# Optimization experiments

Measured on AMD Instinct MI355X. Metric: run time of the kernel, lower is better.

## Reference

```python
import jax, jax.numpy as jnp
import numpy as np

B, T, DIM, H, D = 4, 2048, 1024, 8, 128
HDIM = H * D


def _rope_tables(t, head_dim):
    # angular_freq: (1/1024)^linspace(0,1,D/4) concatenated with D/4 zeros -> length D/2
    freq = (1.0 / 1024.0) ** jnp.linspace(0.0, 1.0, head_dim // 4)
    freq = jnp.concatenate([freq.astype(jnp.float32), jnp.zeros(head_dim // 4, jnp.float32)])
    theta = jnp.arange(t, dtype=jnp.float32)[:, None] * freq[None, :]  # [T, D/2]
    return jnp.cos(theta), jnp.sin(theta)


def _rms_norm(x):
    # F.rms_norm with no weight, default eps = finfo(dtype).eps
    eps = jnp.finfo(jnp.float32).eps
    return x * jax.lax.rsqrt(jnp.mean(x * x, axis=-1, keepdims=True) + eps)


def _rope(x, cos, sin):
    # x: [B,T,H,D]; rotate-half form matching the torch module
    x1, x2 = jnp.split(x, 2, axis=-1)
    c = cos[None, :, None, :]
    s = sin[None, :, None, :]
    return jnp.concatenate([x1 * c + x2 * s, -x1 * s + x2 * c], axis=-1)


def setup_inputs() -> dict:
    key = jax.random.key(0)
    k0, k1, k2, k3 = jax.random.split(key, 4)
    std = 0.5 * DIM ** -0.5
    bound = (3.0 ** 0.5) * std
    x = jax.random.normal(k0, (B, T, DIM), jnp.float32)
    ve = jax.random.normal(k1, (B, T, HDIM), jnp.float32)
    qkv_w = jax.random.uniform(k2, (3, HDIM, DIM), jnp.float32, -bound, bound)
    lambdas = jnp.array([0.5, 0.5], jnp.float32)
    # c_proj is zero-initialized in the module; use small random weight so output is nontrivial
    c_proj_w = jax.random.uniform(k3, (DIM, HDIM), jnp.float32, -bound, bound)
    return {"x": x, "ve": ve, "qkv_w": qkv_w, "lambdas": lambdas, "c_proj_w": c_proj_w}


def reference(x, ve, qkv_w, lambdas, c_proj_w):
    b, t, dim = x.shape
    hdim = qkv_w.shape[1]
    h, d = hdim // 128, 128
    # fused QKV projection (no bias)
    qkv = (x @ qkv_w.reshape(3 * hdim, dim).T).reshape(b, t, 3 * h, d)
    q, k, v = qkv[:, :, :h], qkv[:, :, h:2 * h], qkv[:, :, 2 * h:]
    # QK RMSNorm then RoPE
    q, k = _rms_norm(q), _rms_norm(k)
    cos, sin = _rope_tables(t, d)
    q, k = _rope(q, cos, sin), _rope(k, cos, sin)
    # lambda-weighted value-embedding mix
    v = lambdas[0] * v + lambdas[1] * ve.reshape(b, t, h, d)
    # naive attention with explicit causal mask (masked_fill -1e9)
    scores = jnp.einsum('bqhd,bkhd->bhqk', q, k) * (d ** -0.5)
    causal = jnp.triu(jnp.ones((t, t), bool), k=1)  # True above diagonal
    scores = jnp.where(causal[None, None], jnp.float32(-1e9), scores)
    probs = jax.nn.softmax(scores, axis=-1)
    y = jnp.einsum('bhqk,bkhd->bqhd', probs, v).reshape(b, t, hdim)
    return y @ c_proj_w.T
```

## Files before the change

### kernel.cpp

```cpp
#include <hip/hip_runtime.h>
#include <hip/hip_bf16.h>

constexpr int B_ = 4;
constexpr int T_ = 2048;
constexpr int DIM_ = 1024;
constexpr int H_ = 8;
constexpr int D_ = 128;
constexpr int HDIM_ = H_ * D_;

typedef __attribute__((ext_vector_type(8))) short bf16x8;
typedef __attribute__((ext_vector_type(8))) unsigned short ushort8;
typedef __attribute__((ext_vector_type(4))) float f32x4;

#define ATTN_SCALE 0.08838834764831845f

__device__ __forceinline__ unsigned short f2bf(float x) {
    unsigned u = __float_as_uint(x);
    unsigned r = (u + 0x7FFFu + ((u >> 16) & 1u)) >> 16;
    return (unsigned short)r;
}
__device__ __forceinline__ float bf2f(unsigned short u) {
    return __uint_as_float(((unsigned)u) << 16);
}

__device__ __forceinline__ void async_ld16(void* ldsdst, const void* gsrc) {
    __builtin_amdgcn_global_load_lds(
        (const __attribute__((address_space(1))) unsigned int*)gsrc,
        (__attribute__((address_space(3))) unsigned int*)ldsdst, 16, 0, 0);
}

__global__ __launch_bounds__(256) void cvtk(const float* __restrict__ in,
                                            unsigned short* __restrict__ out, int n4) {
    int i = blockIdx.x * 256 + threadIdx.x;
    if (i < n4) {
        float4 v = ((const float4*)in)[i];
        ushort4 o;
        o.x = f2bf(v.x); o.y = f2bf(v.y); o.z = f2bf(v.z); o.w = f2bf(v.w);
        ((ushort4*)out)[i] = o;
    }
}

__global__ void rope_tables_k(float* __restrict__ cost, float* __restrict__ sint) {
    int idx = blockIdx.x * blockDim.x + threadIdx.x;
    if (idx >= T_ * 32) return;
    int t = idx >> 5, j = idx & 31;
    float e = (float)j * (1.0f / 31.0f);
    float freq = powf(1.0f / 1024.0f, e);
    float th = (float)t * freq;
    cost[idx] = cosf(th);
    sint[idx] = sinf(th);
}

__global__ __launch_bounds__(256) void gemm_bf16_nt(
    const unsigned short* __restrict__ A, const unsigned short* __restrict__ Bw,
    float* __restrict__ Cf, unsigned short* __restrict__ Cb,
    int M, int N, int K) {
    __shared__ __align__(16) unsigned short As[128 * 64];
    __shared__ __align__(16) unsigned short Bs[128 * 64];
    const int tid = threadIdx.x;
    const int l = tid & 63, w = tid >> 6;
    const int g = l >> 4, q16 = l & 15;

    int nwg = gridDim.x * gridDim.y;
    int lin = blockIdx.y * gridDim.x + blockIdx.x;
    int swz = (lin & 7) * (nwg >> 3) + (lin >> 3);
    int bx = swz % gridDim.x, by = swz / gridDim.x;
    const size_t m0 = (size_t)by * 128, n0 = (size_t)bx * 128;
    const int wm = (w >> 1) * 64, wn = (w & 1) * 64;

    f32x4 acc[4][4];
#pragma unroll
    for (int i = 0; i < 4; ++i)
#pragma unroll
        for (int j = 0; j < 4; ++j) acc[i][j] = (f32x4){0.f, 0.f, 0.f, 0.f};

    const int srow = l >> 3;
    const int schunk = (l & 7) ^ (srow & 7);
    const unsigned short* aBase = A + (m0 + srow) * (size_t)K + schunk * 8;
    const unsigned short* bBase = Bw + (n0 + srow) * (size_t)K + schunk * 8;
    const int roff = q16 & 7;

    for (int k0 = 0; k0 < K; k0 += 64) {
#pragma unroll
        for (int i = 0; i < 4; ++i) {
            size_t rstep = (size_t)(w * 4 + i) * 8 * K;
            async_ld16(&As[(w * 4 + i) * 512], aBase + rstep + k0);
            async_ld16(&Bs[(w * 4 + i) * 512], bBase + rstep + k0);
        }
        __syncthreads();
        __builtin_amdgcn_s_setprio(1);
#pragma unroll
        for (int ks = 0; ks < 2; ++ks) {
            bf16x8 af[4], bf[4];
#pragma unroll
            for (int f = 0; f < 4; ++f) {
                int off = (ks * 32 + g * 8) ^ (roff << 3);
                af[f] = *(const bf16x8*)&As[(wm + f * 16 + q16) * 64 + off];
                bf[f] = *(const bf16x8*)&Bs[(wn + f * 16 + q16) * 64 + off];
            }
#pragma unroll
            for (int fm = 0; fm < 4; ++fm)
#pragma unroll
                for (int fn = 0; fn < 4; ++fn)
                    acc[fm][fn] = __builtin_amdgcn_mfma_f32_16x16x32_bf16(
                        af[fm], bf[fn], acc[fm][fn], 0, 0, 0);
        }
        __builtin_amdgcn_s_setprio(0);
        __syncthreads();
    }

    if (Cb) {
#pragma unroll
        for (int fm = 0; fm < 4; ++fm)
#pragma unroll
            for (int r = 0; r < 4; ++r) {
                size_t base = (m0 + wm + fm * 16 + 4 * g + r) * (size_t)N + n0 + wn + q16;
#pragma unroll
                for (int fn = 0; fn < 4; ++fn)
                    Cb[base + fn * 16] = f2bf(acc[fm][fn][r]);
            }
    } else {
#pragma unroll
        for (int fm = 0; fm < 4; ++fm)
#pragma unroll
            for (int r = 0; r < 4; ++r) {
                size_t base = (m0 + wm + fm * 16 + 4 * g + r) * (size_t)N + n0 + wn + q16;
#pragma unroll
                for (int fn = 0; fn < 4; ++fn)
                    Cf[base + fn * 16] = acc[fm][fn][r];
            }
    }
}

__global__ __launch_bounds__(256) void qkv_prep_k(
    unsigned short* __restrict__ qkv,
    const float* __restrict__ cost, const float* __restrict__ sint) {
    const int gw = (blockIdx.x * 256 + threadIdx.x) >> 6;
    const int lane = threadIdx.x & 63;
    const int h = gw & (H_ - 1);
    const int t = (gw / H_) & (T_ - 1);
    const int b = gw / (H_ * T_);
    const size_t rowbase = ((size_t)(b * T_ + t) * 3) * HDIM_ + (size_t)h * D_;
    const float c = (lane < 32) ? cost[t * 32 + lane] : 1.0f;
    const float s = (lane < 32) ? sint[t * 32 + lane] : 0.0f;
    const float EPS = 1.1920928955078125e-07f;

#pragma unroll
    for (int qk = 0; qk < 2; ++qk) {
        unsigned short* p = qkv + rowbase + (size_t)qk * HDIM_;
        float x1 = bf2f(p[lane]), x2 = bf2f(p[lane + 64]);
        float ss = x1 * x1 + x2 * x2;
#pragma unroll
        for (int m = 32; m >= 1; m >>= 1) ss += __shfl_xor(ss, m, 64);
        float r = 1.0f / sqrtf(ss * (1.0f / 128.0f) + EPS);
        x1 *= r; x2 *= r;
        p[lane]      = f2bf(x1 * c + x2 * s);
        p[lane + 64] = f2bf(x2 * c - x1 * s);
    }
}

__global__ __launch_bounds__(256) void vtrans_k(
    const unsigned short* __restrict__ qkv, const float* __restrict__ ve,
    const float* __restrict__ lambdas, unsigned short* __restrict__ vT) {
    __shared__ unsigned short lds[64][65];
    const int tid = threadIdx.x;
    const int d0 = blockIdx.x * 64, t0 = blockIdx.y * 64;
    const int p = blockIdx.z;
    const int h = p & 7, b = p >> 3;
    const float l0 = lambdas[0], l1 = lambdas[1];

#pragma unroll
    for (int u = 0; u < 2; ++u) {
        int unit = tid + u * 256;
        int i = unit >> 3, jc = (unit & 7) * 8;
        size_t row = (size_t)(b * T_ + t0 + i);
        ushort8 vv = *(const ushort8*)&qkv[(row * 3 + 2) * HDIM_ + h * D_ + d0 + jc];
        const float* pe = &ve[row * HDIM_ + h * D_ + d0 + jc];
        float4 e0 = *(const float4*)pe;
        float4 e1 = *(const float4*)(pe + 4);
        lds[i][jc + 0] = f2bf(l0 * bf2f(vv[0]) + l1 * e0.x);
        lds[i][jc + 1] = f2bf(l0 * bf2f(vv[1]) + l1 * e0.y);
        lds[i][jc + 2] = f2bf(l0 * bf2f(vv[2]) + l1 * e0.z);
        lds[i][jc + 3] = f2bf(l0 * bf2f(vv[3]) + l1 * e0.w);
        lds[i][jc + 4] = f2bf(l0 * bf2f(vv[4]) + l1 * e1.x);
        lds[i][jc + 5] = f2bf(l0 * bf2f(vv[5]) + l1 * e1.y);
        lds[i][jc + 6] = f2bf(l0 * bf2f(vv[6]) + l1 * e1.z);
        lds[i][jc + 7] = f2bf(l0 * bf2f(vv[7]) + l1 * e1.w);
    }
    __syncthreads();
#pragma unroll
    for (int u = 0; u < 2; ++u) {
        int unit = tid + u * 256;
        int r = unit >> 3, tc = (unit & 7) * 8;
        ushort8 o;
#pragma unroll
        for (int m = 0; m < 8; ++m) o[m] = lds[tc + m][r];
        *(ushort8*)&vT[((size_t)(b * H_ + h) * D_ + d0 + r) * T_ + t0 + tc] = o;
    }
}

__global__ __launch_bounds__(512, 4) void attn_mfma(
    const unsigned short* __restrict__ qkv, const unsigned short* __restrict__ vT,
    unsigned short* __restrict__ y) {
    __shared__ __align__(16) unsigned short Ks[2][64 * 128];
    __shared__ __align__(16) unsigned short Vs[2][128 * 64];
    __shared__ __align__(16) unsigned short Pt[8][16 * 64];

    const int tid = threadIdx.x;
    const int l = tid & 63, w = tid >> 6;
    const int g = l >> 4, q16 = l & 15;
    const int bid = blockIdx.x;
    const int xcd = bid & 7, slot = bid >> 3;
    const int pord = slot >> 4, qo = slot & 15;
    const int p = pord * 8 + xcd;
    const int h = p & 7, b = p >> 3;
    const int qt = 15 - qo;
    const int q0 = qt * 128;
    const int roff = q16 & 7;

    const int jk0 = w * 2;
    const int krow0 = jk0 * 4 + g,        krow1 = (jk0 + 1) * 4 + g;
    const int kch0  = q16 ^ (krow0 & 7),  kch1  = q16 ^ (krow1 & 7);
    const int vrow0 = jk0 * 8 + (l >> 3), vrow1 = (jk0 + 1) * 8 + (l >> 3);
    const int vch0  = (l & 7) ^ (vrow0 & 7), vch1 = (l & 7) ^ (vrow1 & 7);
    const unsigned short* kp0 =
        &qkv[((size_t)(b * T_ + krow0) * 3 + 1) * HDIM_ + h * D_ + kch0 * 8];
    const unsigned short* kp1 =
        &qkv[((size_t)(b * T_ + krow1) * 3 + 1) * HDIM_ + h * D_ + kch1 * 8];
    const unsigned short* vp0 =
        &vT[((size_t)(b * H_ + h) * D_ + vrow0) * T_ + vch0 * 8];
    const unsigned short* vp1 =
        &vT[((size_t)(b * H_ + h) * D_ + vrow1) * T_ + vch1 * 8];
    const size_t kstep = (size_t)64 * 3 * HDIM_;

#define STAGE_KV(buf, it_) do {                                   \
        size_t ko_ = (size_t)(it_) * kstep; int vo_ = (it_) * 64; \
        async_ld16(&Ks[buf][jk0 * 512],       kp0 + ko_);         \
        async_ld16(&Ks[buf][(jk0 + 1) * 512], kp1 + ko_);         \
        async_ld16(&Vs[buf][jk0 * 512],       vp0 + vo_);         \
        async_ld16(&Vs[buf][(jk0 + 1) * 512], vp1 + vo_);         \
    } while (0)

    const int qrow = q0 + w * 16 + q16;
    const size_t qbase = ((size_t)(b * T_ + qrow) * 3) * HDIM_ + (size_t)h * D_;
    bf16x8 qf[4];
#pragma unroll
    for (int ks = 0; ks < 4; ++ks)
        qf[ks] = *(const bf16x8*)&qkv[qbase + ks * 32 + g * 8];

    f32x4 accO[8];
#pragma unroll
    for (int i = 0; i < 8; ++i) accO[i] = (f32x4){0.f, 0.f, 0.f, 0.f};
    float m_s = -1e30f, l_s = 0.f;

    const int nkv = 2 * qt + 2;
    int cur = 0;
    STAGE_KV(0, 0);

    for (int it = 0; it < nkv; ++it) {
        const int kv0 = it * 64;
        __syncthreads();
        if (it + 1 < nkv) STAGE_KV(cur ^ 1, it + 1);

        f32x4 st[4];
        __builtin_amdgcn_s_setprio(1);
#pragma unroll
        for (int fk = 0; fk < 4; ++fk) {
            f32x4 a = (f32x4){0.f, 0.f, 0.f, 0.f};
            int row = fk * 16 + q16;
#pragma unroll
            for (int ks = 0; ks < 4; ++ks) {
                bf16x8 kf = *(const bf16x8*)&Ks[cur][row * 128 +
                                                ((ks * 32 + g * 8) ^ (roff << 3))];
                a = __builtin_amdgcn_mfma_f32_16x16x32_bf16(kf, qf[ks], a, 0, 0, 0);
            }
            st[fk] = a;
        }
        __builtin_amdgcn_s_setprio(0);

        float sv[4][4];
        float pmax = -1e30f;
        const bool edge = (kv0 + 64 > q0);
#pragma unroll
        for (int fk = 0; fk < 4; ++fk)
#pragma unroll
            for (int r = 0; r < 4; ++r) {
                float sc_ = st[fk][r] * ATTN_SCALE;
                if (edge) {
                    int kvg = kv0 + fk * 16 + 4 * g + r;
                    if (kvg > qrow) sc_ = -1e30f;
                }
                sv[fk][r] = sc_;
                pmax = fmaxf(pmax, sc_);
            }
        pmax = fmaxf(pmax, __shfl_xor(pmax, 16));
        pmax = fmaxf(pmax, __shfl_xor(pmax, 32));

        if (!__all(pmax - m_s <= 8.0f)) {
            float mnew = fmaxf(m_s, pmax);
            float scl = __expf(m_s - mnew);
            m_s = mnew;
            l_s *= scl;
            f32x4 scv;
            scv[0] = __shfl(scl, 4 * g + 0);
            scv[1] = __shfl(scl, 4 * g + 1);
            scv[2] = __shfl(scl, 4 * g + 2);
            scv[3] = __shfl(scl, 4 * g + 3);
#pragma unroll
            for (int fo = 0; fo < 8; ++fo) accO[fo] *= scv;
        }

        float rsum = 0.f;
#pragma unroll
        for (int fk = 0; fk < 4; ++fk)
#pragma unroll
            for (int r = 0; r < 4; ++r) {
                sv[fk][r] = __expf(sv[fk][r] - m_s);
                rsum += sv[fk][r];
            }
        rsum += __shfl_xor(rsum, 16);
        rsum += __shfl_xor(rsum, 32);
        l_s += rsum;

#pragma unroll
        for (int fk = 0; fk < 4; ++fk) {
            unsigned long long pk =
                (unsigned long long)f2bf(sv[fk][0])        |
                ((unsigned long long)f2bf(sv[fk][1]) << 16) |
                ((unsigned long long)f2bf(sv[fk][2]) << 32) |
                ((unsigned long long)f2bf(sv[fk][3]) << 48);
            int kv = fk * 16 + 4 * g;
            *(unsigned long long*)&Pt[w][q16 * 64 + (kv ^ (roff << 3))] = pk;
        }

        bf16x8 pa[2];
#pragma unroll
        for (int ks = 0; ks < 2; ++ks)
            pa[ks] = *(const bf16x8*)&Pt[w][q16 * 64 + ((ks * 32 + g * 8) ^ (roff << 3))];
        __builtin_amdgcn_s_setprio(1);
#pragma unroll
        for (int fo = 0; fo < 8; ++fo) {
            int drow = fo * 16 + q16;
#pragma unroll
            for (int ks = 0; ks < 2; ++ks) {
                bf16x8 vf = *(const bf16x8*)&Vs[cur][drow * 64 +
                                                ((ks * 32 + g * 8) ^ (roff << 3))];
                accO[fo] = __builtin_amdgcn_mfma_f32_16x16x32_bf16(pa[ks], vf, accO[fo], 0, 0, 0);
            }
        }
        __builtin_amdgcn_s_setprio(0);
        cur ^= 1;
    }
#undef STAGE_KV

    float inv = 1.0f / l_s;
    f32x4 iv;
    iv[0] = __shfl(inv, 4 * g + 0);
    iv[1] = __shfl(inv, 4 * g + 1);
    iv[2] = __shfl(inv, 4 * g + 2);
    iv[3] = __shfl(inv, 4 * g + 3);
#pragma unroll
    for (int r = 0; r < 4; ++r) {
        size_t yb = ((size_t)(b * T_ + q0 + w * 16 + 4 * g + r)) * HDIM_ +
                    (size_t)h * D_ + q16;
#pragma unroll
        for (int fo = 0; fo < 8; ++fo)
            y[yb + fo * 16] = f2bf(accO[fo][r] * iv[r]);
    }
}

extern "C" void kernel_launch(void* const* d_in, const int* in_sizes, int n_in,
                              void* d_out, int out_size, void* d_ws, size_t ws_size,
                              hipStream_t stream) {
    (void)in_sizes; (void)n_in; (void)out_size; (void)ws_size;
    const float* x        = (const float*)d_in[0];
    const float* ve       = (const float*)d_in[1];
    const float* qkv_w    = (const float*)d_in[2];
    const float* lambdas  = (const float*)d_in[3];
    const float* c_proj_w = (const float*)d_in[4];
    float* out = (float*)d_out;

    char* ws = (char*)d_ws;
    unsigned short* qkv = (unsigned short*)ws;
    unsigned short* y   = (unsigned short*)(ws + 50331648);
    unsigned short* xb  = (unsigned short*)(ws + 67108864);
    unsigned short* wb  = (unsigned short*)(ws + 83886080);
    unsigned short* pb  = (unsigned short*)(ws + 90177536);
    float* cost = (float*)(ws + 92274688);
    float* sint = cost + T_ * 32;
    unsigned short* vT  = (unsigned short*)(ws + 100663296);

    hipLaunchKernelGGL(cvtk, dim3(8192), dim3(256), 0, stream, x, xb, 8192 * 1024 / 4);
    hipLaunchKernelGGL(cvtk, dim3(3072), dim3(256), 0, stream, qkv_w, wb, 3072 * 1024 / 4);
    hipLaunchKernelGGL(cvtk, dim3(1024), dim3(256), 0, stream, c_proj_w, pb, 1024 * 1024 / 4);
    hipLaunchKernelGGL(rope_tables_k, dim3(256), dim3(256), 0, stream, cost, sint);

    hipLaunchKernelGGL(gemm_bf16_nt, dim3(24, 64), dim3(256), 0, stream,
                       xb, wb, (float*)nullptr, qkv, B_ * T_, 3 * HDIM_, DIM_);
    hipLaunchKernelGGL(qkv_prep_k, dim3(B_ * T_ * H_ / 4), dim3(256), 0, stream,
                       qkv, cost, sint);
    hipLaunchKernelGGL(vtrans_k, dim3(2, 32, 32), dim3(256), 0, stream,
                       qkv, ve, lambdas, vT);
    hipLaunchKernelGGL(attn_mfma, dim3(512), dim3(512), 0, stream, qkv, vT, y);
    hipLaunchKernelGGL(gemm_bf16_nt, dim3(8, 64), dim3(256), 0, stream,
                       y, pb, out, (unsigned short*)nullptr, B_ * T_, DIM_, HDIM_);
}
```

Measured before the change: 340.2 us.

## Switch attention to 32x32x16 MFMA with register-shuffled P and 4-wave blocks

Rewrites the attention kernel to use 32x32x16 bf16 MFMA tiles, with 4 waves of 32 query rows each instead of 8 waves of 16. The P matrix is kept in registers via cross-half-wave shuffles rather than staged through LDS, so the Pt buffer and its LDS round trip go away. Row statistics now need fewer shuffles, and outputs are written as vectorised ushort4 stores. The query-tile order is also alternated across block groups to balance causal work. In exchange, register pressure per thread is higher and each block has fewer waves for latency hiding.

```diff
diff --git a/kernel.cpp b/kernel.cpp
--- a/kernel.cpp
+++ b/kernel.cpp
@@ -11,6 +11,7 @@
 typedef __attribute__((ext_vector_type(8))) short bf16x8;
 typedef __attribute__((ext_vector_type(8))) unsigned short ushort8;
 typedef __attribute__((ext_vector_type(4))) float f32x4;
+typedef __attribute__((ext_vector_type(16))) float f32x16;
 
 #define ATTN_SCALE 0.08838834764831845f
 
@@ -199,58 +200,54 @@
     }
 }
 
-__global__ __launch_bounds__(512, 4) void attn_mfma(
+__global__ __launch_bounds__(256, 2) void attn_mfma(
     const unsigned short* __restrict__ qkv, const unsigned short* __restrict__ vT,
     unsigned short* __restrict__ y) {
     __shared__ __align__(16) unsigned short Ks[2][64 * 128];
     __shared__ __align__(16) unsigned short Vs[2][128 * 64];
-    __shared__ __align__(16) unsigned short Pt[8][16 * 64];
 
     const int tid = threadIdx.x;
     const int l = tid & 63, w = tid >> 6;
-    const int g = l >> 4, q16 = l & 15;
+    const int l31 = l & 31, hi = l >> 5, l7 = l & 7;
     const int bid = blockIdx.x;
     const int xcd = bid & 7, slot = bid >> 3;
     const int pord = slot >> 4, qo = slot & 15;
     const int p = pord * 8 + xcd;
     const int h = p & 7, b = p >> 3;
-    const int qt = 15 - qo;
+    const int qt = (pord < 2) ? (15 - qo) : qo;
     const int q0 = qt * 128;
-    const int roff = q16 & 7;
-
-    const int jk0 = w * 2;
-    const int krow0 = jk0 * 4 + g,        krow1 = (jk0 + 1) * 4 + g;
-    const int kch0  = q16 ^ (krow0 & 7),  kch1  = q16 ^ (krow1 & 7);
-    const int vrow0 = jk0 * 8 + (l >> 3), vrow1 = (jk0 + 1) * 8 + (l >> 3);
-    const int vch0  = (l & 7) ^ (vrow0 & 7), vch1 = (l & 7) ^ (vrow1 & 7);
-    const unsigned short* kp0 =
-        &qkv[((size_t)(b * T_ + krow0) * 3 + 1) * HDIM_ + h * D_ + kch0 * 8];
-    const unsigned short* kp1 =
-        &qkv[((size_t)(b * T_ + krow1) * 3 + 1) * HDIM_ + h * D_ + kch1 * 8];
-    const unsigned short* vp0 =
-        &vT[((size_t)(b * H_ + h) * D_ + vrow0) * T_ + vch0 * 8];
-    const unsigned short* vp1 =
-        &vT[((size_t)(b * H_ + h) * D_ + vrow1) * T_ + vch1 * 8];
-    const size_t kstep = (size_t)64 * 3 * HDIM_;
-
-#define STAGE_KV(buf, it_) do {                                   \
-        size_t ko_ = (size_t)(it_) * kstep; int vo_ = (it_) * 64; \
-        async_ld16(&Ks[buf][jk0 * 512],       kp0 + ko_);         \
-        async_ld16(&Ks[buf][(jk0 + 1) * 512], kp1 + ko_);         \
-        async_ld16(&Vs[buf][jk0 * 512],       vp0 + vo_);         \
-        async_ld16(&Vs[buf][(jk0 + 1) * 512], vp1 + vo_);         \
+
+    const unsigned short* kp[4];
+    const unsigned short* vp[4];
+#pragma unroll
+    for (int i = 0; i < 4; ++i) {
+        int r = 16 * w + 4 * i + (l >> 4);
+        int kch = (l & 15) ^ (r & 7);
+        kp[i] = &qkv[((size_t)(b * T_ + r) * 3 + 1) * HDIM_ + h * D_ + kch * 8];
+        int d = 32 * w + 8 * i + (l >> 3);
+        int vch = l7 ^ (d & 7);
+        vp[i] = &vT[((size_t)(b * H_ + h) * D_ + d) * T_ + vch * 8];
+    }
+#define STAGE_KV(buf, it_) do {                                        \
+        size_t ko_ = (size_t)(it_) * (64 * 3 * HDIM_);                 \
+        int vo_ = (it_) * 64;                                          \
+        _Pragma("unroll")                                              \
+        for (int i_ = 0; i_ < 4; ++i_) {                               \
+            async_ld16(&Ks[buf][(w * 4 + i_) * 512], kp[i_] + ko_);    \
+            async_ld16(&Vs[buf][(w * 4 + i_) * 512], vp[i_] + vo_);    \
+        }                                                              \
     } while (0)
 
-    const int qrow = q0 + w * 16 + q16;
-    const size_t qbase = ((size_t)(b * T_ + qrow) * 3) * HDIM_ + (size_t)h * D_;
-    bf16x8 qf[4];
-#pragma unroll
-    for (int ks = 0; ks < 4; ++ks)
-        qf[ks] = *(const bf16x8*)&qkv[qbase + ks * 32 + g * 8];
-
-    f32x4 accO[8];
-#pragma unroll
-    for (int i = 0; i < 8; ++i) accO[i] = (f32x4){0.f, 0.f, 0.f, 0.f};
+    const int qc = q0 + w * 32 + l31;
+    const size_t qbase = ((size_t)(b * T_ + qc) * 3) * HDIM_ + (size_t)h * D_;
+    bf16x8 qf[8];
+#pragma unroll
+    for (int ks = 0; ks < 8; ++ks)
+        qf[ks] = *(const bf16x8*)&qkv[qbase + ks * 16 + hi * 8];
+
+    f32x16 accO[4];
+#pragma unroll
+    for (int i = 0; i < 4; ++i) accO[i] = (f32x16)(0.f);
     float m_s = -1e30f, l_s = 0.f;
 
     const int nkv = 2 * qt + 2;
@@ -262,38 +259,37 @@
         __syncthreads();
         if (it + 1 < nkv) STAGE_KV(cur ^ 1, it + 1);
 
-        f32x4 st[4];
+        f32x16 st[2];
         __builtin_amdgcn_s_setprio(1);
 #pragma unroll
-        for (int fk = 0; fk < 4; ++fk) {
-            f32x4 a = (f32x4){0.f, 0.f, 0.f, 0.f};
-            int row = fk * 16 + q16;
-#pragma unroll
-            for (int ks = 0; ks < 4; ++ks) {
+        for (int mt = 0; mt < 2; ++mt) {
+            f32x16 a = (f32x16)(0.f);
+            int row = mt * 32 + l31;
+#pragma unroll
+            for (int ks = 0; ks < 8; ++ks) {
                 bf16x8 kf = *(const bf16x8*)&Ks[cur][row * 128 +
-                                                ((ks * 32 + g * 8) ^ (roff << 3))];
-                a = __builtin_amdgcn_mfma_f32_16x16x32_bf16(kf, qf[ks], a, 0, 0, 0);
-            }
-            st[fk] = a;
+                                                     8 * ((2 * ks + hi) ^ l7)];
+                a = __builtin_amdgcn_mfma_f32_32x32x16_bf16(kf, qf[ks], a, 0, 0, 0);
+            }
+            st[mt] = a;
         }
         __builtin_amdgcn_s_setprio(0);
 
-        float sv[4][4];
+        float sv[2][16];
         float pmax = -1e30f;
         const bool edge = (kv0 + 64 > q0);
 #pragma unroll
-        for (int fk = 0; fk < 4; ++fk)
-#pragma unroll
-            for (int r = 0; r < 4; ++r) {
-                float sc_ = st[fk][r] * ATTN_SCALE;
+        for (int mt = 0; mt < 2; ++mt)
+#pragma unroll
+            for (int r = 0; r < 16; ++r) {
+                float x = st[mt][r] * ATTN_SCALE;
                 if (edge) {
-                    int kvg = kv0 + fk * 16 + 4 * g + r;
-                    if (kvg > qrow) sc_ = -1e30f;
+                    int kvg = kv0 + 32 * mt + (r & 3) + 8 * (r >> 2) + 4 * hi;
+                    if (kvg > qc) x = -1e30f;
                 }
-                sv[fk][r] = sc_;
-                pmax = fmaxf(pmax, sc_);
-            }
-        pmax = fmaxf(pmax, __shfl_xor(pmax, 16));
+                sv[mt][r] = x;
+                pmax = fmaxf(pmax, x);
+            }
         pmax = fmaxf(pmax, __shfl_xor(pmax, 32));
 
         if (!__all(pmax - m_s <= 8.0f)) {
@@ -301,51 +297,58 @@
             float scl = __expf(m_s - mnew);
             m_s = mnew;
             l_s *= scl;
-            f32x4 scv;
-            scv[0] = __shfl(scl, 4 * g + 0);
-            scv[1] = __shfl(scl, 4 * g + 1);
-            scv[2] = __shfl(scl, 4 * g + 2);
-            scv[3] = __shfl(scl, 4 * g + 3);
-#pragma unroll
-            for (int fo = 0; fo < 8; ++fo) accO[fo] *= scv;
+#pragma unroll
+            for (int dt = 0; dt < 4; ++dt) accO[dt] *= scl;
         }
 
         float rsum = 0.f;
 #pragma unroll
-        for (int fk = 0; fk < 4; ++fk)
-#pragma unroll
-            for (int r = 0; r < 4; ++r) {
-                sv[fk][r] = __expf(sv[fk][r] - m_s);
-                rsum += sv[fk][r];
-            }
-        rsum += __shfl_xor(rsum, 16);
+        for (int mt = 0; mt < 2; ++mt)
+#pragma unroll
+            for (int r = 0; r < 16; ++r) {
+                sv[mt][r] = __expf(sv[mt][r] - m_s);
+                rsum += sv[mt][r];
+            }
         rsum += __shfl_xor(rsum, 32);
         l_s += rsum;
 
-#pragma unroll
-        for (int fk = 0; fk < 4; ++fk) {
-            unsigned long long pk =
-                (unsigned long long)f2bf(sv[fk][0])        |
-                ((unsigned long long)f2bf(sv[fk][1]) << 16) |
-                ((unsigned long long)f2bf(sv[fk][2]) << 32) |
-                ((unsigned long long)f2bf(sv[fk][3]) << 48);
-            int kv = fk * 16 + 4 * g;
-            *(unsigned long long*)&Pt[w][q16 * 64 + (kv ^ (roff << 3))] = pk;
-        }
-
-        bf16x8 pa[2];
-#pragma unroll
-        for (int ks = 0; ks < 2; ++ks)
-            pa[ks] = *(const bf16x8*)&Pt[w][q16 * 64 + ((ks * 32 + g * 8) ^ (roff << 3))];
+        bf16x8 pb[4];
+#pragma unroll
+        for (int mt = 0; mt < 2; ++mt) {
+            unsigned w0[4], w1[4], sw0[4], sw1[4];
+#pragma unroll
+            for (int s = 0; s < 4; ++s) {
+                w0[s] = (unsigned)f2bf(sv[mt][4 * s + 0]) |
+                        ((unsigned)f2bf(sv[mt][4 * s + 1]) << 16);
+                w1[s] = (unsigned)f2bf(sv[mt][4 * s + 2]) |
+                        ((unsigned)f2bf(sv[mt][4 * s + 3]) << 16);
+            }
+#pragma unroll
+            for (int s = 0; s < 4; ++s) {
+                sw0[s] = __shfl_xor(w0[s], 32);
+                sw1[s] = __shfl_xor(w1[s], 32);
+            }
+#pragma unroll
+            for (int ktl = 0; ktl < 2; ++ktl) {
+                union { unsigned u[4]; bf16x8 v; } pu;
+                pu.u[0] = hi ? sw0[2 * ktl + 1] : w0[2 * ktl];
+                pu.u[1] = hi ? sw1[2 * ktl + 1] : w1[2 * ktl];
+                pu.u[2] = hi ? w0[2 * ktl + 1] : sw0[2 * ktl];
+                pu.u[3] = hi ? w1[2 * ktl + 1] : sw1[2 * ktl];
+                pb[mt * 2 + ktl] = pu.v;
+            }
+        }
+
         __builtin_amdgcn_s_setprio(1);
 #pragma unroll
-        for (int fo = 0; fo < 8; ++fo) {
-            int drow = fo * 16 + q16;
-#pragma unroll
-            for (int ks = 0; ks < 2; ++ks) {
+        for (int dt = 0; dt < 4; ++dt) {
+            int drow = dt * 32 + l31;
+#pragma unroll
+            for (int kt = 0; kt < 4; ++kt) {
                 bf16x8 vf = *(const bf16x8*)&Vs[cur][drow * 64 +
-                                                ((ks * 32 + g * 8) ^ (roff << 3))];
-                accO[fo] = __builtin_amdgcn_mfma_f32_16x16x32_bf16(pa[ks], vf, accO[fo], 0, 0, 0);
+                                                     8 * ((2 * kt + hi) ^ l7)];
+                accO[dt] = __builtin_amdgcn_mfma_f32_32x32x16_bf16(vf, pb[kt],
+                                                                   accO[dt], 0, 0, 0);
             }
         }
         __builtin_amdgcn_s_setprio(0);
@@ -354,19 +357,18 @@
 #undef STAGE_KV
 
     float inv = 1.0f / l_s;
-    f32x4 iv;
-    iv[0] = __shfl(inv, 4 * g + 0);
-    iv[1] = __shfl(inv, 4 * g + 1);
-    iv[2] = __shfl(inv, 4 * g + 2);
-    iv[3] = __shfl(inv, 4 * g + 3);
-#pragma unroll
-    for (int r = 0; r < 4; ++r) {
-        size_t yb = ((size_t)(b * T_ + q0 + w * 16 + 4 * g + r)) * HDIM_ +
-                    (size_t)h * D_ + q16;
-#pragma unroll
-        for (int fo = 0; fo < 8; ++fo)
-            y[yb + fo * 16] = f2bf(accO[fo][r] * iv[r]);
-    }
+    const size_t yb = (size_t)(b * T_ + qc) * HDIM_ + (size_t)h * D_;
+#pragma unroll
+    for (int dt = 0; dt < 4; ++dt)
+#pragma unroll
+        for (int s = 0; s < 4; ++s) {
+            ushort4 o;
+            o.x = f2bf(accO[dt][4 * s + 0] * inv);
+            o.y = f2bf(accO[dt][4 * s + 1] * inv);
+            o.z = f2bf(accO[dt][4 * s + 2] * inv);
+            o.w = f2bf(accO[dt][4 * s + 3] * inv);
+            *(ushort4*)&y[yb + dt * 32 + 8 * s + 4 * hi] = o;
+        }
 }
 
 extern "C" void kernel_launch(void* const* d_in, const int* in_sizes, int n_in,
@@ -401,7 +403,7 @@
                        qkv, cost, sint);
     hipLaunchKernelGGL(vtrans_k, dim3(2, 32, 32), dim3(256), 0, stream,
                        qkv, ve, lambdas, vT);
-    hipLaunchKernelGGL(attn_mfma, dim3(512), dim3(512), 0, stream, qkv, vT, y);
+    hipLaunchKernelGGL(attn_mfma, dim3(512), dim3(256), 0, stream, qkv, vT, y);
     hipLaunchKernelGGL(gemm_bf16_nt, dim3(8, 64), dim3(256), 0, stream,
                        y, pb, out, (unsigned short*)nullptr, B_ * T_, DIM_, HDIM_);
 }
```

Measured after the change: 332.1 us. 2.4% less time.
